# Optimization experiments

Measured on AMD Instinct MI355X. Metric: run time of the kernel, lower is better.

The kernel has to match this reference:

```python
import jax, jax.numpy as jnp
import numpy as np

HEADS = 16


def _linear(x, w, b):
    # torch nn.Linear: y = x @ W^T + b, W: (out, in)
    return jnp.einsum('bld,od->blo', x, w) + b


def setup_inputs() -> dict:
    key = jax.random.key(0)
    ks = jax.random.split(key, 11)
    B, L, QD, KVD = 8, 2048, 1024, 1024
    s_in = 1.0 / np.sqrt(QD)
    return {
        'query': jax.random.normal(ks[0], (B, L, QD), jnp.float32),
        'key':   jax.random.normal(ks[1], (B, L, KVD), jnp.float32),
        'value': jax.random.normal(ks[2], (B, L, KVD), jnp.float32),
        'wq_w': jax.random.normal(ks[3], (KVD, QD), jnp.float32) * s_in,
        'wq_b': jnp.zeros((KVD,), jnp.float32),
        'wk_w': jax.random.normal(ks[4], (KVD, KVD), jnp.float32) * s_in,
        'wk_b': jnp.zeros((KVD,), jnp.float32),
        'wv_w': jax.random.normal(ks[5], (KVD, KVD), jnp.float32) * s_in,
        'wv_b': jnp.zeros((KVD,), jnp.float32),
        'fo_w': jax.random.normal(ks[6], (QD, KVD), jnp.float32) * s_in,
        'fo_b': jnp.zeros((QD,), jnp.float32),
    }


def reference(query, key, value, wq_w, wq_b, wk_w, wk_b, wv_w, wv_b, fo_w, fo_b):
    B, Lq, _ = query.shape
    Lk = key.shape[1]
    kvd = wq_w.shape[0]
    head_dim = kvd // HEADS
    # reshape WITHOUT transpose, exactly as the torch source: (B, L, heads, head_dim)
    q = _linear(query, wq_w, wq_b).reshape(B, Lq, HEADS, head_dim)
    k = _linear(key,   wk_w, wk_b).reshape(B, Lk, HEADS, head_dim)
    v = _linear(value, wv_w, wv_b).reshape(B, Lk, HEADS, head_dim)
    scale = 1.0 / jnp.sqrt(jnp.float32(head_dim))
    # Faithful to source: seq axis acts as 'h'; heads axis is contracted (i,j).
    scores = jnp.einsum('bhid,bhjd->bhij', q, k) * scale  # (B, L, heads, heads)
    weights = jax.nn.softmax(scores, axis=-1)
    out = jnp.einsum('bhij,bhjd->bhid', weights, v)       # (B, L, heads, head_dim)
    out = out.reshape(B, Lq, kvd)
    return _linear(out, fo_w, fo_b)
```

## Files before the change

### kernel.cpp

```cpp
#include <hip/hip_runtime.h>
#include <hip/hip_bf16.h>


typedef __attribute__((ext_vector_type(8))) __bf16 bf16x8;
typedef __attribute__((ext_vector_type(4))) float f32x4;

#define BM 128
#define BN 128
#define BK 64

__device__ __forceinline__ float bf2f(ushort u) {
  union { unsigned int i; float f; } c; c.i = ((unsigned int)u) << 16; return c.f;
}
__device__ __forceinline__ ushort f2b(float f) {
  union { float f; unsigned int i; } c; c.f = f;
  unsigned int x = c.i;
  return (ushort)((x + 0x7FFFu + ((x >> 16) & 1u)) >> 16);
}

__global__ __launch_bounds__(256)
void cvt_f32_bf16(const float* __restrict__ s, ushort* __restrict__ d, int n8)
{
  int i = blockIdx.x * 256 + threadIdx.x;
  if (i >= n8) return;
  const float4* sp = reinterpret_cast<const float4*>(s) + (size_t)i * 2;
  float4 a = sp[0], b = sp[1];
  ushort u[8] = { f2b(a.x), f2b(a.y), f2b(a.z), f2b(a.w),
                  f2b(b.x), f2b(b.y), f2b(b.z), f2b(b.w) };
  reinterpret_cast<uint4*>(d)[i] = *reinterpret_cast<uint4*>(u);
}

__global__ __launch_bounds__(256)
void cvt_in3(const float* __restrict__ a, const float* __restrict__ b,
             const float* __restrict__ c, ushort* __restrict__ dst, int n8each)
{
  int i = blockIdx.x * 256 + threadIdx.x;
  if (i >= 3 * n8each) return;
  const float* s; int j;
  if (i < n8each)          { s = a; j = i; }
  else if (i < 2 * n8each) { s = b; j = i - n8each; }
  else                     { s = c; j = i - 2 * n8each; }
  const float4* sp = reinterpret_cast<const float4*>(s) + (size_t)j * 2;
  float4 x = sp[0], y = sp[1];
  ushort u[8] = { f2b(x.x), f2b(x.y), f2b(x.z), f2b(x.w),
                  f2b(y.x), f2b(y.y), f2b(y.z), f2b(y.w) };
  reinterpret_cast<uint4*>(dst)[i] = *reinterpret_cast<uint4*>(u);
}

__global__ __launch_bounds__(256)
void cvt_w3(const float* __restrict__ a, const float* __restrict__ b,
            const float* __restrict__ c, ushort* __restrict__ dst, int n8each)
{
  int i = blockIdx.x * 256 + threadIdx.x;
  if (i >= 3 * n8each) return;
  const float* s; int j;
  if (i < n8each)          { s = a; j = i; }
  else if (i < 2 * n8each) { s = b; j = i - n8each; }
  else                     { s = c; j = i - 2 * n8each; }
  const float4* sp = reinterpret_cast<const float4*>(s) + (size_t)j * 2;
  float4 x = sp[0], y = sp[1];
  ushort u[8] = { f2b(x.x), f2b(x.y), f2b(x.z), f2b(x.w),
                  f2b(y.x), f2b(y.y), f2b(y.z), f2b(y.w) };
  reinterpret_cast<uint4*>(dst)[i] = *reinterpret_cast<uint4*>(u);
}

__global__ __launch_bounds__(256)
void cvt_wo_perm(const float* __restrict__ w, ushort* __restrict__ o)
{
  int t = blockIdx.x * 256 + threadIdx.x;
  int n  = t >> 7;
  int i8 = (t & 127) << 3;
  int blk = i8 >> 8, g = (i8 >> 6) & 3, c = (i8 >> 2) & 15;
  const float* src = w + (size_t)n * 1024 + 4 * g * 64 + blk * 16 + c;
  ushort u[8];
  #pragma unroll
  for (int j = 0; j < 8; ++j)
    u[j] = f2b(src[(j & 3) * 64 + (j >> 2)]);
  *reinterpret_cast<uint4*>(o + (size_t)n * 1024 + i8) = *reinterpret_cast<uint4*>(u);
}

template<int CMODE>
__device__ __forceinline__
void gemm_body(const ushort* __restrict__ A, const ushort* __restrict__ Bw,
               const float* __restrict__ bias, void* __restrict__ Cv,
               int N, int K, ushort* lds)
{
  const int tid  = threadIdx.x;
  const int lane = tid & 63;
  const int wid  = tid >> 6;
  const int wm   = wid >> 2;
  const int wn   = wid & 3;

  const int nwg = gridDim.x * gridDim.y;
  int fid = blockIdx.y * gridDim.x + blockIdx.x;
  if ((nwg & 7) == 0) fid = (fid & 7) * (nwg >> 3) + (fid >> 3);
  const int bx = fid % gridDim.x;
  const int by = fid / gridDim.x;
  const int m0 = by * 256, n0 = bx * 256;

  const int NT = K >> 6;

  const int csw = ((lane & 7) ^ (lane >> 3)) << 3;
  auto STAGE = [&](int h, int kt, int b) {
    const ushort* base = (h >= 2) ? Bw : A;
    const int o0 = (h >= 2) ? n0 : m0;
    const int rl = (h & 1) * 128;
    #pragma unroll
    for (int j = 0; j < 2; ++j) {
      int rt = rl + j * 64 + wid * 8;
      const ushort* src = base + (size_t)(o0 + rt + (lane >> 3)) * K + kt * 64 + csw;
      ushort* dst = lds + b * 32768 + (h >= 2 ? 16384 : 0) + rt * 64;
      __builtin_amdgcn_global_load_lds(
          (const __attribute__((address_space(1))) void*)src,
          (__attribute__((address_space(3))) void*)dst, 16, 0, 0);
    }
  };

  auto LDA = [&](int b, int mi, int kk) -> bf16x8 {
    int row  = (mi & 3) * 16 + wm * 64 + (mi >> 2) * 128 + (lane & 15);
    int slot = kk * 4 + (lane >> 4);
    int byte = row * 128 + (((slot ^ (row & 7)) & 7) << 4);
    return *reinterpret_cast<const bf16x8*>((const char*)(lds + b * 32768) + byte);
  };
  auto LDB = [&](int b, int ni, int kk) -> bf16x8 {
    int row  = (ni & 1) * 16 + wn * 32 + (ni >> 1) * 128 + (lane & 15);
    int slot = kk * 4 + (lane >> 4);
    int byte = row * 128 + (((slot ^ (row & 7)) & 7) << 4);
    return *reinterpret_cast<const bf16x8*>((const char*)(lds + b * 32768 + 16384) + byte);
  };

  f32x4 acc[8][4] = {};
  bf16x8 af[4][2], bf[4][2];

  STAGE(0, 0, 0); STAGE(2, 0, 0); STAGE(3, 0, 0); STAGE(1, 0, 0);
  asm volatile("s_waitcnt vmcnt(4)" ::: "memory");
  __builtin_amdgcn_s_barrier();

  for (int t = 0; t < NT; ++t) {
    const int cur = t & 1;
    const int nxt = cur ^ 1;
    const bool pf = (t + 1) < NT;

    #pragma unroll
    for (int i = 0; i < 4; ++i) { af[i][0] = LDA(cur, i, 0); af[i][1] = LDA(cur, i, 1); }
    #pragma unroll
    for (int n = 0; n < 2; ++n) { bf[n][0] = LDB(cur, n, 0); bf[n][1] = LDB(cur, n, 1); }
    if (pf) { STAGE(0, t + 1, nxt); asm volatile("s_waitcnt vmcnt(4)" ::: "memory"); }
    else    {                       asm volatile("s_waitcnt vmcnt(2)" ::: "memory"); }
    __builtin_amdgcn_s_barrier();
    asm volatile("s_waitcnt lgkmcnt(0)" ::: "memory");
    __builtin_amdgcn_sched_barrier(0);
    __builtin_amdgcn_s_setprio(1);
    #pragma unroll
    for (int i = 0; i < 4; ++i)
      #pragma unroll
      for (int n = 0; n < 2; ++n)
        #pragma unroll
        for (int kk = 0; kk < 2; ++kk)
          acc[i][n] = __builtin_amdgcn_mfma_f32_16x16x32_bf16(af[i][kk], bf[n][kk], acc[i][n], 0, 0, 0);
    __builtin_amdgcn_s_setprio(0);
    __builtin_amdgcn_s_barrier();

    #pragma unroll
    for (int n = 0; n < 2; ++n) { bf[2 + n][0] = LDB(cur, 2 + n, 0); bf[2 + n][1] = LDB(cur, 2 + n, 1); }
    if (pf) { STAGE(2, t + 1, nxt); asm volatile("s_waitcnt vmcnt(4)" ::: "memory"); }
    else    {                       asm volatile("s_waitcnt vmcnt(0)" ::: "memory"); }
    __builtin_amdgcn_s_barrier();
    asm volatile("s_waitcnt lgkmcnt(0)" ::: "memory");
    __builtin_amdgcn_sched_barrier(0);
    __builtin_amdgcn_s_setprio(1);
    #pragma unroll
    for (int i = 0; i < 4; ++i)
      #pragma unroll
      for (int n = 0; n < 2; ++n)
        #pragma unroll
        for (int kk = 0; kk < 2; ++kk)
          acc[i][2 + n] = __builtin_amdgcn_mfma_f32_16x16x32_bf16(af[i][kk], bf[2 + n][kk], acc[i][2 + n], 0, 0, 0);
    __builtin_amdgcn_s_setprio(0);
    __builtin_amdgcn_s_barrier();

    #pragma unroll
    for (int i = 0; i < 4; ++i) { af[i][0] = LDA(cur, 4 + i, 0); af[i][1] = LDA(cur, 4 + i, 1); }
    if (pf) STAGE(3, t + 1, nxt);
    __builtin_amdgcn_s_barrier();
    asm volatile("s_waitcnt lgkmcnt(0)" ::: "memory");
    __builtin_amdgcn_sched_barrier(0);
    __builtin_amdgcn_s_setprio(1);
    #pragma unroll
    for (int i = 0; i < 4; ++i)
      #pragma unroll
      for (int n = 0; n < 2; ++n)
        #pragma unroll
        for (int kk = 0; kk < 2; ++kk)
          acc[4 + i][n] = __builtin_amdgcn_mfma_f32_16x16x32_bf16(af[i][kk], bf[n][kk], acc[4 + i][n], 0, 0, 0);
    __builtin_amdgcn_s_setprio(0);
    __builtin_amdgcn_s_barrier();

    if (pf) { STAGE(1, t + 1, nxt); asm volatile("s_waitcnt vmcnt(4)" ::: "memory"); }
    __builtin_amdgcn_s_barrier();
    __builtin_amdgcn_s_setprio(1);
    #pragma unroll
    for (int i = 0; i < 4; ++i)
      #pragma unroll
      for (int n = 0; n < 2; ++n)
        #pragma unroll
        for (int kk = 0; kk < 2; ++kk)
          acc[4 + i][2 + n] = __builtin_amdgcn_mfma_f32_16x16x32_bf16(af[i][kk], bf[2 + n][kk], acc[4 + i][2 + n], 0, 0, 0);
    __builtin_amdgcn_s_setprio(0);
    __builtin_amdgcn_s_barrier();
  }

  #pragma unroll
  for (int ni = 0; ni < 4; ++ni) {
    int col = n0 + (ni & 1) * 16 + wn * 32 + (ni >> 1) * 128 + (lane & 15);
    float bv = bias[col];
    #pragma unroll
    for (int mi = 0; mi < 8; ++mi) {
      int row0 = m0 + (mi & 3) * 16 + wm * 64 + (mi >> 2) * 128 + ((lane >> 4) << 2);
      #pragma unroll
      for (int q = 0; q < 4; ++q) {
        float v = acc[mi][ni][q] + bv;
        if constexpr (CMODE == 0)
          ((float*)Cv)[(size_t)(row0 + q) * N + col] = v;
        else
          ((ushort*)Cv)[(size_t)(row0 + q) * N + col] = f2b(v);
      }
    }
  }
}

template<int CMODE>
__global__ __launch_bounds__(512, 2)
void gemm8p(const ushort* __restrict__ A, const ushort* __restrict__ Bw,
            const float* __restrict__ bias, void* __restrict__ Cv,
            int M, int N, int K)
{
  extern __shared__ ushort lds[];
  gemm_body<CMODE>(A, Bw, bias, Cv, N, K, lds);
}

__global__ __launch_bounds__(512, 2)
void gemm8p_qkv(const ushort* __restrict__ Abase, const ushort* __restrict__ Wbase,
                const float* __restrict__ b0, const float* __restrict__ b1,
                const float* __restrict__ b2, ushort* __restrict__ Cbase,
                int M, int N, int K)
{
  extern __shared__ ushort lds[];
  const int z = blockIdx.z;
  const size_t slot = (size_t)M * K;
  const size_t wsl  = (size_t)N * K;
  const float* bias = (z == 0) ? b0 : (z == 1) ? b1 : b2;
  gemm_body<1>(Abase + z * slot, Wbase + z * wsl, bias,
               (void*)(Cbase + z * (size_t)M * N), N, K, lds);
}

__global__ __launch_bounds__(256)
void attn_mfma2(const ushort* __restrict__ Q, const ushort* __restrict__ Kh,
                const ushort* __restrict__ V, ushort* __restrict__ Ot, int P)
{
  const int lane = threadIdx.x & 63;
  const int wid  = threadIdx.x >> 6;
  const int g = lane >> 4, c = lane & 15;
  const int stride = gridDim.x * 4;

  for (int p = blockIdx.x * 4 + wid; p < P; p += stride) {
    const ushort* qb = Q  + (size_t)p * 1024;
    const ushort* kb = Kh + (size_t)p * 1024;
    const ushort* vb = V  + (size_t)p * 1024;

    bf16x8 qf0 = *reinterpret_cast<const bf16x8*>(qb + c * 64 + g * 8);
    bf16x8 qf1 = *reinterpret_cast<const bf16x8*>(qb + c * 64 + 32 + g * 8);
    bf16x8 kf0 = *reinterpret_cast<const bf16x8*>(kb + c * 64 + g * 8);
    bf16x8 kf1 = *reinterpret_cast<const bf16x8*>(kb + c * 64 + 32 + g * 8);

    f32x4 s = {};
    s = __builtin_amdgcn_mfma_f32_16x16x32_bf16(kf0, qf0, s, 0, 0, 0);
    s = __builtin_amdgcn_mfma_f32_16x16x32_bf16(kf1, qf1, s, 0, 0, 0);

    float s0 = s[0] * 0.125f, s1 = s[1] * 0.125f;
    float s2 = s[2] * 0.125f, s3 = s[3] * 0.125f;
    float m = fmaxf(fmaxf(s0, s1), fmaxf(s2, s3));
    m = fmaxf(m, __shfl_xor(m, 16));
    m = fmaxf(m, __shfl_xor(m, 32));
    float e0 = __expf(s0 - m), e1 = __expf(s1 - m);
    float e2 = __expf(s2 - m), e3 = __expf(s3 - m);
    float sum = e0 + e1 + e2 + e3;
    sum += __shfl_xor(sum, 16);
    sum += __shfl_xor(sum, 32);
    float r = 1.0f / sum;

    uint pk0 = (uint)f2b(e0 * r) | ((uint)f2b(e1 * r) << 16);
    uint pk1 = (uint)f2b(e2 * r) | ((uint)f2b(e3 * r) << 16);

    int srcA = (((2 * g) & 3) << 4) | c;
    int srcB = (((2 * g + 1) & 3) << 4) | c;
    uint a0 = (uint)__shfl((int)pk0, srcA);
    uint a1 = (uint)__shfl((int)pk1, srcA);
    uint a2 = (uint)__shfl((int)pk0, srcB);
    uint a3 = (uint)__shfl((int)pk1, srcB);
    if (g >= 2) { a0 = 0; a1 = 0; a2 = 0; a3 = 0; }
    union { uint u[4]; bf16x8 v; } pa;
    pa.u[0] = a0; pa.u[1] = a1; pa.u[2] = a2; pa.u[3] = a3;

    ushort* ob = Ot + (size_t)p * 1024;
    #pragma unroll
    for (int blk = 0; blk < 4; ++blk) {
      union { ushort u[8]; bf16x8 v; } vf;
      #pragma unroll
      for (int e = 0; e < 8; ++e)
        vf.u[e] = vb[(8 * (g & 1) + e) * 64 + blk * 16 + c];
      f32x4 o = {};
      o = __builtin_amdgcn_mfma_f32_16x16x32_bf16(pa.v, vf.v, o, 0, 0, 0);
      uint lo = (uint)f2b(o[0]) | ((uint)f2b(o[1]) << 16);
      uint hi = (uint)f2b(o[2]) | ((uint)f2b(o[3]) << 16);
      uint2 w2; w2.x = lo; w2.y = hi;
      *reinterpret_cast<uint2*>(ob + blk * 256 + g * 64 + c * 4) = w2;
    }
  }
}

template<bool A_IS_BF16, bool OUT_BF16>
__global__ __launch_bounds__(256)
void gemm_bt(const void* __restrict__ Av, const float* __restrict__ B,
             const float* __restrict__ bias, void* __restrict__ Cv,
             int M, int N, int K)
{
  __shared__ ushort As[BM * BK];
  __shared__ ushort Bs[BN * BK];

  const int tid  = threadIdx.x;
  const int lane = tid & 63;
  const int wid  = tid >> 6;
  const int wr   = wid >> 1;
  const int wc   = wid & 1;
  const int m0   = blockIdx.y * BM;
  const int n0   = blockIdx.x * BN;

  f32x4 acc[4][4] = {};

  const int r   = tid >> 1;
  const int seg = (tid & 1) * 32;

  for (int k0 = 0; k0 < K; k0 += BK) {
    {
      ushort tmp[32];
      if constexpr (A_IS_BF16) {
        const ushort* gA = (const ushort*)Av + (size_t)(m0 + r) * K + k0 + seg;
        #pragma unroll
        for (int u = 0; u < 4; ++u)
          *reinterpret_cast<uint4*>(&tmp[u * 8]) =
              *reinterpret_cast<const uint4*>(gA + u * 8);
      } else {
        const float* gA = (const float*)Av + (size_t)(m0 + r) * K + k0 + seg;
        #pragma unroll
        for (int u = 0; u < 8; ++u) {
          float4 f = *reinterpret_cast<const float4*>(gA + u * 4);
          tmp[u * 4 + 0] = f2b(f.x); tmp[u * 4 + 1] = f2b(f.y);
          tmp[u * 4 + 2] = f2b(f.z); tmp[u * 4 + 3] = f2b(f.w);
        }
      }
      #pragma unroll
      for (int s4 = 0; s4 < 4; ++s4) {
        int slot = (seg >> 3) + s4;
        int byte = r * 128 + ((slot ^ (r & 7)) << 4);
        *reinterpret_cast<uint4*>((char*)As + byte) =
            *reinterpret_cast<uint4*>(&tmp[s4 * 8]);
      }
    }
    {
      const float* gB = B + (size_t)(n0 + r) * K + k0 + seg;
      ushort tmp[32];
      #pragma unroll
      for (int u = 0; u < 8; ++u) {
        float4 f = *reinterpret_cast<const float4*>(gB + u * 4);
        tmp[u * 4 + 0] = f2b(f.x); tmp[u * 4 + 1] = f2b(f.y);
        tmp[u * 4 + 2] = f2b(f.z); tmp[u * 4 + 3] = f2b(f.w);
      }
      #pragma unroll
      for (int s4 = 0; s4 < 4; ++s4) {
        int slot = (seg >> 3) + s4;
        int byte = r * 128 + ((slot ^ (r & 7)) << 4);
        *reinterpret_cast<uint4*>((char*)Bs + byte) =
            *reinterpret_cast<uint4*>(&tmp[s4 * 8]);
      }
    }
    __syncthreads();

    #pragma unroll
    for (int kk = 0; kk < 2; ++kk) {
      const int kbase = kk * 32 + ((lane >> 4) << 3);
      const int slot  = kbase >> 3;
      bf16x8 af[4], bfr[4];
      #pragma unroll
      for (int mi = 0; mi < 4; ++mi) {
        int row = wr * 64 + mi * 16 + (lane & 15);
        af[mi] = *reinterpret_cast<const bf16x8*>(
            (const char*)As + row * 128 + ((slot ^ (row & 7)) << 4));
      }
      #pragma unroll
      for (int ni = 0; ni < 4; ++ni) {
        int row = wc * 64 + ni * 16 + (lane & 15);
        bfr[ni] = *reinterpret_cast<const bf16x8*>(
            (const char*)Bs + row * 128 + ((slot ^ (row & 7)) << 4));
      }
      #pragma unroll
      for (int mi = 0; mi < 4; ++mi)
        #pragma unroll
        for (int ni = 0; ni < 4; ++ni)
          acc[mi][ni] = __builtin_amdgcn_mfma_f32_16x16x32_bf16(
              af[mi], bfr[ni], acc[mi][ni], 0, 0, 0);
    }
    __syncthreads();
  }

  #pragma unroll
  for (int ni = 0; ni < 4; ++ni) {
    int col = n0 + wc * 64 + ni * 16 + (lane & 15);
    float bv = bias[col];
    #pragma unroll
    for (int mi = 0; mi < 4; ++mi) {
      int row0 = m0 + wr * 64 + mi * 16 + ((lane >> 4) << 2);
      #pragma unroll
      for (int q = 0; q < 4; ++q) {
        float v = acc[mi][ni][q] + bv;
        if constexpr (OUT_BF16)
          ((ushort*)Cv)[(size_t)(row0 + q) * N + col] = f2b(v);
        else
          ((float*)Cv)[(size_t)(row0 + q) * N + col] = v;
      }
    }
  }
}

__global__ __launch_bounds__(256)
void attn_kernel(const ushort* __restrict__ Q, const ushort* __restrict__ Kh,
                 const ushort* __restrict__ V, ushort* __restrict__ O)
{
  __shared__ float smem[4][3][16][68];
  const int tid  = threadIdx.x;
  const int wid  = tid >> 6;
  const int lane = tid & 63;
  const size_t p = (size_t)blockIdx.x * 4 + wid;

  {
    const ushort* srcs[3] = { Q + p * 1024, Kh + p * 1024, V + p * 1024 };
    const int i  = lane >> 2;
    const int d0 = (lane & 3) * 16;
    #pragma unroll
    for (int m = 0; m < 3; ++m) {
      const ushort* s = srcs[m] + lane * 16;
      ushort u[16];
      *reinterpret_cast<uint4*>(&u[0]) = *reinterpret_cast<const uint4*>(s);
      *reinterpret_cast<uint4*>(&u[8]) = *reinterpret_cast<const uint4*>(s + 8);
      #pragma unroll
      for (int e = 0; e < 16; ++e) smem[wid][m][i][d0 + e] = bf2f(u[e]);
    }
  }
  __syncthreads();

  const int i  = lane >> 2;
  const int jg = lane & 3;
  const float* qrow = smem[wid][0][i];
  const float* k0r = smem[wid][1][jg * 4 + 0];
  const float* k1r = smem[wid][1][jg * 4 + 1];
  const float* k2r = smem[wid][1][jg * 4 + 2];
  const float* k3r = smem[wid][1][jg * 4 + 3];

  float s0 = 0.f, s1 = 0.f, s2 = 0.f, s3 = 0.f;
  #pragma unroll
  for (int d = 0; d < 64; ++d) {
    float qv = qrow[d];
    s0 += qv * k0r[d]; s1 += qv * k1r[d];
    s2 += qv * k2r[d]; s3 += qv * k3r[d];
  }
  const float scale = 0.125f;
  s0 *= scale; s1 *= scale; s2 *= scale; s3 *= scale;

  float mx = fmaxf(fmaxf(s0, s1), fmaxf(s2, s3));
  mx = fmaxf(mx, __shfl_xor(mx, 1));
  mx = fmaxf(mx, __shfl_xor(mx, 2));
  float e0 = __expf(s0 - mx), e1 = __expf(s1 - mx);
  float e2 = __expf(s2 - mx), e3 = __expf(s3 - mx);
  float sum = e0 + e1 + e2 + e3;
  sum += __shfl_xor(sum, 1);
  sum += __shfl_xor(sum, 2);
  float inv = 1.0f / sum;
  e0 *= inv; e1 *= inv; e2 *= inv; e3 *= inv;

  const float* v0r = smem[wid][2][jg * 4 + 0];
  const float* v1r = smem[wid][2][jg * 4 + 1];
  const float* v2r = smem[wid][2][jg * 4 + 2];
  const float* v3r = smem[wid][2][jg * 4 + 3];
  ushort* orow = O + p * 1024 + i * 64;

  #pragma unroll
  for (int cc = 0; cc < 4; ++cc) {
    float po[16];
    #pragma unroll
    for (int dd = 0; dd < 16; ++dd) {
      int d = cc * 16 + dd;
      po[dd] = e0 * v0r[d] + e1 * v1r[d] + e2 * v2r[d] + e3 * v3r[d];
    }
    #pragma unroll
    for (int dd = 0; dd < 16; ++dd) {
      po[dd] += __shfl_xor(po[dd], 1);
      po[dd] += __shfl_xor(po[dd], 2);
    }
    if (jg == cc) {
      #pragma unroll
      for (int dd = 0; dd < 16; ++dd) orow[cc * 16 + dd] = f2b(po[dd]);
    }
  }
}

extern "C" void kernel_launch(void* const* d_in, const int* in_sizes, int n_in,
                              void* d_out, int out_size, void* d_ws, size_t ws_size,
                              hipStream_t stream)
{
  const float* query = (const float*)d_in[0];
  const float* key_  = (const float*)d_in[1];
  const float* value = (const float*)d_in[2];
  const float* wq_w  = (const float*)d_in[3];
  const float* wq_b  = (const float*)d_in[4];
  const float* wk_w  = (const float*)d_in[5];
  const float* wk_b  = (const float*)d_in[6];
  const float* wv_w  = (const float*)d_in[7];
  const float* wv_b  = (const float*)d_in[8];
  const float* fo_w  = (const float*)d_in[9];
  const float* fo_b  = (const float*)d_in[10];

  const int K = 1024, N = 1024;
  const int M = in_sizes[0] / K;
  const size_t slot = (size_t)M * N;
  const size_t wsl  = (size_t)N * K;
  const size_t need_big = (6 * slot + 4 * wsl) * sizeof(ushort);
  const size_t need_mid = (4 * slot + 4 * wsl) * sizeof(ushort);
  const bool dims_ok = (M % 256) == 0 && N == 1024 && K == 1024;

  const int n8w = (int)(wsl / 8);
  const int n8s = (int)(slot / 8);

  if (ws_size >= need_big && dims_ok) {
    hipFuncSetAttribute(reinterpret_cast<const void*>(gemm8p<0>),
                        hipFuncAttributeMaxDynamicSharedMemorySize, 131072);
    hipFuncSetAttribute(reinterpret_cast<const void*>(gemm8p_qkv),
                        hipFuncAttributeMaxDynamicSharedMemorySize, 131072);

    ushort* I0 = (ushort*)d_ws;
    ushort* P1 = I0 + 3 * slot;
    ushort* Wq = P1 + 3 * slot;
    ushort* Wo = Wq + 3 * wsl;
    ushort* Ot = I0;

    dim3 g8(N / 256, M / 256);
    dim3 g8z(N / 256, M / 256, 3);
    dim3 b8(512);

    cvt_w3<<<dim3((3 * n8w + 255) / 256), dim3(256), 0, stream>>>(
        wq_w, wk_w, wv_w, Wq, n8w);
    cvt_wo_perm<<<dim3(512), dim3(256), 0, stream>>>(fo_w, Wo);
    cvt_in3<<<dim3((3 * n8s + 255) / 256), dim3(256), 0, stream>>>(
        query, key_, value, I0, n8s);

    gemm8p_qkv<<<g8z, b8, 131072, stream>>>(I0, Wq, wq_b, wk_b, wv_b, P1, M, N, K);

    attn_mfma2<<<dim3(2048), dim3(256), 0, stream>>>(
        P1, P1 + slot, P1 + 2 * slot, Ot, M);
    gemm8p<0><<<g8, b8, 131072, stream>>>(Ot, Wo, fo_b, d_out, M, N, K);
  } else if (ws_size >= need_mid && dims_ok) {
    hipFuncSetAttribute(reinterpret_cast<const void*>(gemm8p<0>),
                        hipFuncAttributeMaxDynamicSharedMemorySize, 131072);
    hipFuncSetAttribute(reinterpret_cast<const void*>(gemm8p<1>),
                        hipFuncAttributeMaxDynamicSharedMemorySize, 131072);

    ushort* S0 = (ushort*)d_ws;
    ushort* S1 = S0 + slot;
    ushort* S2 = S1 + slot;
    ushort* S3 = S2 + slot;
    ushort* Wq = S3 + slot;
    ushort* Wo = Wq + 3 * wsl;

    dim3 g8(N / 256, M / 256);
    dim3 b8(512);

    cvt_w3<<<dim3((3 * n8w + 255) / 256), dim3(256), 0, stream>>>(
        wq_w, wk_w, wv_w, Wq, n8w);
    cvt_wo_perm<<<dim3(512), dim3(256), 0, stream>>>(fo_w, Wo);

    cvt_f32_bf16<<<dim3((n8s + 255) / 256), dim3(256), 0, stream>>>(query, S0, n8s);
    gemm8p<1><<<g8, b8, 131072, stream>>>(S0, Wq,           wq_b, S1, M, N, K);
    cvt_f32_bf16<<<dim3((n8s + 255) / 256), dim3(256), 0, stream>>>(key_, S0, n8s);
    gemm8p<1><<<g8, b8, 131072, stream>>>(S0, Wq + wsl,     wk_b, S2, M, N, K);
    cvt_f32_bf16<<<dim3((n8s + 255) / 256), dim3(256), 0, stream>>>(value, S0, n8s);
    gemm8p<1><<<g8, b8, 131072, stream>>>(S0, Wq + 2 * wsl, wv_b, S3, M, N, K);

    attn_mfma2<<<dim3(2048), dim3(256), 0, stream>>>(S1, S2, S3, S0, M);
    gemm8p<0><<<g8, b8, 131072, stream>>>(S0, Wo, fo_b, d_out, M, N, K);
  } else {
    dim3 grid(N / BN, M / BM);
    ushort* Qb = (ushort*)d_ws;
    ushort* Kb = Qb + slot;
    ushort* Vb = Kb + slot;
    ushort* Ob = Vb + slot;
    gemm_bt<false, true><<<grid, dim3(256), 0, stream>>>(query, wq_w, wq_b, Qb, M, N, K);
    gemm_bt<false, true><<<grid, dim3(256), 0, stream>>>(key_,  wk_w, wk_b, Kb, M, N, K);
    gemm_bt<false, true><<<grid, dim3(256), 0, stream>>>(value, wv_w, wv_b, Vb, M, N, K);
    attn_kernel<<<dim3(M / 4), dim3(256), 0, stream>>>(Qb, Kb, Vb, Ob);
    gemm_bt<true, false><<<grid, dim3(256), 0, stream>>>(Ob, fo_w, fo_b, d_out, M, N, K);
  }
}
```

Baseline: 242.5 us.

## Deepen GEMM global prefetch and split weight conversion into per-matrix launches

The GEMM main loop now issues global-to-LDS loads for the next tile earlier: the quarter-stages for tile t+1 go out at the start of the iteration, and those for tile t+2 go out at the end, into the buffer just consumed. The vmcnt waits are retuned to match. The aim is more load latency in flight during the MFMA work, at the cost of tighter waitcnt bookkeeping and a risk of overwriting LDS that is still being read. The fused three-weight conversion kernel is replaced by separate cvt_f32_bf16 launches per weight. This adds launches, and the first launch uses an oversized grid.

```diff
diff --git a/kernel.cpp b/kernel.cpp
--- a/kernel.cpp
+++ b/kernel.cpp
@@ -33,23 +33,6 @@
 __global__ __launch_bounds__(256)
 void cvt_in3(const float* __restrict__ a, const float* __restrict__ b,
              const float* __restrict__ c, ushort* __restrict__ dst, int n8each)
-{
-  int i = blockIdx.x * 256 + threadIdx.x;
-  if (i >= 3 * n8each) return;
-  const float* s; int j;
-  if (i < n8each)          { s = a; j = i; }
-  else if (i < 2 * n8each) { s = b; j = i - n8each; }
-  else                     { s = c; j = i - 2 * n8each; }
-  const float4* sp = reinterpret_cast<const float4*>(s) + (size_t)j * 2;
-  float4 x = sp[0], y = sp[1];
-  ushort u[8] = { f2b(x.x), f2b(x.y), f2b(x.z), f2b(x.w),
-                  f2b(y.x), f2b(y.y), f2b(y.z), f2b(y.w) };
-  reinterpret_cast<uint4*>(dst)[i] = *reinterpret_cast<uint4*>(u);
-}
-
-__global__ __launch_bounds__(256)
-void cvt_w3(const float* __restrict__ a, const float* __restrict__ b,
-            const float* __restrict__ c, ushort* __restrict__ dst, int n8each)
 {
   int i = blockIdx.x * 256 + threadIdx.x;
   if (i >= 3 * n8each) return;
@@ -133,20 +116,21 @@
   bf16x8 af[4][2], bf[4][2];
 
   STAGE(0, 0, 0); STAGE(2, 0, 0); STAGE(3, 0, 0); STAGE(1, 0, 0);
-  asm volatile("s_waitcnt vmcnt(4)" ::: "memory");
+  STAGE(0, 1, 1); STAGE(2, 1, 1);
+  asm volatile("s_waitcnt vmcnt(8)" ::: "memory");
   __builtin_amdgcn_s_barrier();
 
   for (int t = 0; t < NT; ++t) {
     const int cur = t & 1;
     const int nxt = cur ^ 1;
-    const bool pf = (t + 1) < NT;
 
     #pragma unroll
     for (int i = 0; i < 4; ++i) { af[i][0] = LDA(cur, i, 0); af[i][1] = LDA(cur, i, 1); }
     #pragma unroll
     for (int n = 0; n < 2; ++n) { bf[n][0] = LDB(cur, n, 0); bf[n][1] = LDB(cur, n, 1); }
-    if (pf) { STAGE(0, t + 1, nxt); asm volatile("s_waitcnt vmcnt(4)" ::: "memory"); }
-    else    {                       asm volatile("s_waitcnt vmcnt(2)" ::: "memory"); }
+    if (t + 1 < NT) { STAGE(3, t + 1, nxt); STAGE(1, t + 1, nxt);
+                      asm volatile("s_waitcnt vmcnt(8)" ::: "memory"); }
+    else            { asm volatile("s_waitcnt vmcnt(2)" ::: "memory"); }
     __builtin_amdgcn_s_barrier();
     asm volatile("s_waitcnt lgkmcnt(0)" ::: "memory");
     __builtin_amdgcn_sched_barrier(0);
@@ -163,8 +147,7 @@
 
     #pragma unroll
     for (int n = 0; n < 2; ++n) { bf[2 + n][0] = LDB(cur, 2 + n, 0); bf[2 + n][1] = LDB(cur, 2 + n, 1); }
-    if (pf) { STAGE(2, t + 1, nxt); asm volatile("s_waitcnt vmcnt(4)" ::: "memory"); }
-    else    {                       asm volatile("s_waitcnt vmcnt(0)" ::: "memory"); }
+    if (t + 1 >= NT) asm volatile("s_waitcnt vmcnt(0)" ::: "memory");
     __builtin_amdgcn_s_barrier();
     asm volatile("s_waitcnt lgkmcnt(0)" ::: "memory");
     __builtin_amdgcn_sched_barrier(0);
@@ -181,7 +164,6 @@
 
     #pragma unroll
     for (int i = 0; i < 4; ++i) { af[i][0] = LDA(cur, 4 + i, 0); af[i][1] = LDA(cur, 4 + i, 1); }
-    if (pf) STAGE(3, t + 1, nxt);
     __builtin_amdgcn_s_barrier();
     asm volatile("s_waitcnt lgkmcnt(0)" ::: "memory");
     __builtin_amdgcn_sched_barrier(0);
@@ -196,7 +178,9 @@
     __builtin_amdgcn_s_setprio(0);
     __builtin_amdgcn_s_barrier();
 
-    if (pf) { STAGE(1, t + 1, nxt); asm volatile("s_waitcnt vmcnt(4)" ::: "memory"); }
+    if (t + 2 < NT)      { STAGE(0, t + 2, cur); STAGE(2, t + 2, cur);
+                           asm volatile("s_waitcnt vmcnt(8)" ::: "memory"); }
+    else if (t + 1 < NT) { asm volatile("s_waitcnt vmcnt(4)" ::: "memory"); }
     __builtin_amdgcn_s_barrier();
     __builtin_amdgcn_s_setprio(1);
     #pragma unroll
@@ -556,11 +540,13 @@
     dim3 g8z(N / 256, M / 256, 3);
     dim3 b8(512);
 
-    cvt_w3<<<dim3((3 * n8w + 255) / 256), dim3(256), 0, stream>>>(
-        wq_w, wk_w, wv_w, Wq, n8w);
-    cvt_wo_perm<<<dim3(512), dim3(256), 0, stream>>>(fo_w, Wo);
     cvt_in3<<<dim3((3 * n8s + 255) / 256), dim3(256), 0, stream>>>(
         query, key_, value, I0, n8s);
+    cvt_f32_bf16<<<dim3((3 * n8w + 255) / 256), dim3(256), 0, stream>>>(
+        wq_w, (ushort*)nullptr == nullptr ? Wq : Wq, n8w);
+    cvt_f32_bf16<<<dim3((n8w + 255) / 256), dim3(256), 0, stream>>>(wk_w, Wq + wsl, n8w);
+    cvt_f32_bf16<<<dim3((n8w + 255) / 256), dim3(256), 0, stream>>>(wv_w, Wq + 2 * wsl, n8w);
+    cvt_wo_perm<<<dim3(512), dim3(256), 0, stream>>>(fo_w, Wo);
 
     gemm8p_qkv<<<g8z, b8, 131072, stream>>>(I0, Wq, wq_b, wk_b, wv_b, P1, M, N, K);
 
@@ -583,8 +569,9 @@
     dim3 g8(N / 256, M / 256);
     dim3 b8(512);
 
-    cvt_w3<<<dim3((3 * n8w + 255) / 256), dim3(256), 0, stream>>>(
-        wq_w, wk_w, wv_w, Wq, n8w);
+    cvt_f32_bf16<<<dim3((n8w + 255) / 256), dim3(256), 0, stream>>>(wq_w, Wq, n8w);
+    cvt_f32_bf16<<<dim3((n8w + 255) / 256), dim3(256), 0, stream>>>(wk_w, Wq + wsl, n8w);
+    cvt_f32_bf16<<<dim3((n8w + 255) / 256), dim3(256), 0, stream>>>(wv_w, Wq + 2 * wsl, n8w);
     cvt_wo_perm<<<dim3(512), dim3(256), 0, stream>>>(fo_w, Wo);
 
     cvt_f32_bf16<<<dim3((n8s + 255) / 256), dim3(256), 0, stream>>>(query, S0, n8s);
```

New measurement: 236.6 us. 1.02x faster.
